# Kernel tuning notes

Hardware: AMD Instinct MI355X
Metric: run time of the kernel (lower is better)

Reference implementation:

```python
import jax, jax.numpy as jnp
import numpy as np

N_POOL = 500_000   # number of source neurons (value store size)
N_W = 1024         # number of unique (deduplicated) weight matrices
E = 1_000_000      # number of connections (neuron-input pairs)
D_IN = 16
D_OUT = 16


def setup_inputs() -> dict:
    key = jax.random.key(0)
    k1, k2, k3, k4 = jax.random.split(key, 4)
    values = jax.random.normal(k1, (N_POOL, D_IN), dtype=jnp.float32)
    weight = jax.random.normal(k2, (N_W, D_OUT, D_IN), dtype=jnp.float32)
    input_idx = jax.random.randint(k3, (E,), 0, N_POOL, dtype=jnp.int64) if jax.config.jax_enable_x64 else jax.random.randint(k3, (E,), 0, N_POOL).astype(jnp.int32)
    weight_idx = jax.random.randint(k4, (E,), 0, N_W).astype(jnp.int32)
    return {"values": values, "weight": weight, "input_idx": input_idx, "weight_idx": weight_idx}


def reference(values, weight, input_idx, weight_idx):
    # LINEAR_GATHER: gather input value vectors per connection  -> [E, D_IN]
    x = values[input_idx]
    # LINEAR_WEIGHTS_GATHER: gather weight matrices per connection -> [E, D_OUT, D_IN]
    w = weight[weight_idx]
    # LINEAR_LINEAR: per-connection matmul (w @ input_values) -> [E, D_OUT]
    y = jnp.einsum('eoi,ei->eo', w, x)
    return y
```

## Files before the change

### kernel.cpp

```cpp
#include <hip/hip_runtime.h>
#include <hip/hip_fp16.h>


#define D 16
#define WPB 4
#define TPB (WPB * 64)
#define MAXBLK 2048

typedef _Float16 h2v __attribute__((ext_vector_type(2)));

__global__ __launch_bounds__(256) void linear_gather_mv(
    const float* __restrict__ values, const float* __restrict__ weight,
    const int* __restrict__ input_idx, const int* __restrict__ weight_idx,
    float* __restrict__ out, int E)
{
    int tid = blockIdx.x * blockDim.x + threadIdx.x;
    int e = tid >> 2;
    int j = tid & 3;
    if (e >= E) return;
    int ii = input_idx[e];
    int wi = weight_idx[e];
    const float4* xp = (const float4*)(values + (long long)ii * D);
    float4 x0 = xp[0], x1 = xp[1], x2 = xp[2], x3 = xp[3];
    const float4* wp = (const float4*)(weight + (long long)wi * (D * D) + j * (4 * D));
    float4 acc;
    float* accp = (float*)&acc;
    #pragma unroll
    for (int r = 0; r < 4; ++r) {
        float4 w0 = wp[r * 4 + 0], w1 = wp[r * 4 + 1], w2 = wp[r * 4 + 2], w3 = wp[r * 4 + 3];
        accp[r] = w0.x * x0.x + w0.y * x0.y + w0.z * x0.z + w0.w * x0.w
                + w1.x * x1.x + w1.y * x1.y + w1.z * x1.z + w1.w * x1.w
                + w2.x * x2.x + w2.y * x2.y + w2.z * x2.z + w2.w * x2.w
                + w3.x * x3.x + w3.y * x3.y + w3.z * x3.z + w3.w * x3.w;
    }
    ((float4*)out)[(long long)e * 4 + j] = acc;
}

__global__ __launch_bounds__(256) void wconv(
    const float* __restrict__ w, __half* __restrict__ wh, int n)
{
    int i = (blockIdx.x * 256 + threadIdx.x) * 4;
    if (i + 3 >= n) {
        for (int k = i; k < n; ++k) wh[k] = __float2half(w[k]);
        return;
    }
    float4 v = *(const float4*)(w + i);
    __half2 a = __floats2half2_rn(v.x, v.y);
    __half2 b = __floats2half2_rn(v.z, v.w);
    float2 packed;
    ((__half2*)&packed)[0] = a;
    ((__half2*)&packed)[1] = b;
    *(float2*)(wh + i) = packed;
}

#define WPAIR(K, W0, W1) do {                                                  \
    int a0 = __builtin_amdgcn_readlane(wcur, 4*(K)+0);                         \
    int a1 = __builtin_amdgcn_readlane(wcur, 4*(K)+1);                         \
    int a2 = __builtin_amdgcn_readlane(wcur, 4*(K)+2);                         \
    int a3 = __builtin_amdgcn_readlane(wcur, 4*(K)+3);                         \
    W0 = ((const float4*)(wh + (long long)(lh ? a1 : a0) * (D*D)))[hrow];      \
    W1 = ((const float4*)(wh + (long long)(lh ? a3 : a2) * (D*D)))[hrow];      \
} while (0)

#define STEP(CC, WV) do {                                                      \
    int c  = (CC) + lh;                                                        \
    float4 xv = *(const float4*)(xh + (size_t)c * D + (h << 3));               \
    const h2v* xp2 = (const h2v*)&xv;                                          \
    const h2v* wp2 = (const h2v*)&(WV);                                        \
    float p = __builtin_amdgcn_fdot2(wp2[0], xp2[0], 0.0f, false);             \
    p = __builtin_amdgcn_fdot2(wp2[1], xp2[1], p, false);                      \
    p = __builtin_amdgcn_fdot2(wp2[2], xp2[2], p, false);                      \
    p = __builtin_amdgcn_fdot2(wp2[3], xp2[3], p, false);                      \
    p += __shfl_xor(p, 1);            \
    if (h == 0) yh[c * D + rr] = (_Float16)p;                                  \
} while (0)

#define COMP4(K, W0, W1) do { STEP(4*(K)+0, W0); STEP(4*(K)+2, W1); } while (0)

#define IDXLOAD(BI, IV, WV) do {                                               \
    int kl = (BI) * 64 + lane; if (kl >= E) kl = E - 1;                        \
    IV = iidx[kl];                                                             \
    WV = widx[kl];                                                             \
} while (0)

#define XLOAD(IV) do {                                                         \
    int iiu;                                                                   \
    iiu = __shfl(IV,      g4); xq0 = ((const float4*)(values + (long long)iiu * D))[q]; \
    iiu = __shfl(IV, 16 + g4); xq1 = ((const float4*)(values + (long long)iiu * D))[q]; \
    iiu = __shfl(IV, 32 + g4); xq2 = ((const float4*)(values + (long long)iiu * D))[q]; \
    iiu = __shfl(IV, 48 + g4); xq3 = ((const float4*)(values + (long long)iiu * D))[q]; \
} while (0)

#define COMMIT(U, XQ) do {                                                     \
    __half2 c0 = __floats2half2_rn((XQ).x, (XQ).y);                            \
    __half2 c1 = __floats2half2_rn((XQ).z, (XQ).w);                            \
    float2 pk;                                                                 \
    ((__half2*)&pk)[0] = c0;                                                   \
    ((__half2*)&pk)[1] = c1;                                                   \
    *(float2*)(xh + ((U)*16 + g4) * D + (q << 2)) = pk;                        \
} while (0)

__global__ __launch_bounds__(TPB, 4) void direct_mv(
    const float* __restrict__ values, const __half* __restrict__ wh,
    const int* __restrict__ iidx, const int* __restrict__ widx,
    float* __restrict__ out, int E)
{
    __shared__ _Float16 xh_all[WPB * 64 * D];
    __shared__ _Float16 yh_all[WPB * 64 * D];
    const int lane = threadIdx.x & 63;
    const int wid  = threadIdx.x >> 6;
    _Float16* xh = xh_all + wid * (64 * D);
    _Float16* yh = yh_all + wid * (64 * D);
    const int g4 = lane >> 2;
    const int q  = lane & 3;
    const int lh   = lane >> 5;
    const int h    = lane & 1;
    const int hrow = lane & 31;
    const int rr   = (lane & 31) >> 1;

    const int nbatch = (E + 63) >> 6;
    const int gw = blockIdx.x * WPB + wid;
    const int GW = gridDim.x * WPB;
    if (gw >= nbatch) return;

    int ivC, wvC, ivN, wvN;
    float4 xq0, xq1, xq2, xq3;
    IDXLOAD(gw, ivC, wvC);
    XLOAD(ivC);
    if (gw + GW < nbatch) IDXLOAD(gw + GW, ivN, wvN);
    else { ivN = ivC; wvN = wvC; }

    for (int bi = gw; bi < nbatch; bi += GW) {
        COMMIT(0, xq0);
        COMMIT(1, xq1);
        COMMIT(2, xq2);
        COMMIT(3, xq3);
        int wcur = wvC;
        int k0 = bi * 64;
        int nb = E - k0; if (nb > 64) nb = 64;
        float* outb = out + (long long)k0 * D;

        int bn = bi + GW;
        if (bn < nbatch) XLOAD(ivN);
        int bn2 = bi + 2 * GW;
        if (bn2 < nbatch) IDXLOAD(bn2, ivC, wvC);

        float4 P0, P1, Q0, Q1;
        WPAIR( 0, P0, P1);
        WPAIR( 1, Q0, Q1);
        COMP4( 0, P0, P1); WPAIR( 2, P0, P1);
        COMP4( 1, Q0, Q1); WPAIR( 3, Q0, Q1);
        COMP4( 2, P0, P1); WPAIR( 4, P0, P1);
        COMP4( 3, Q0, Q1); WPAIR( 5, Q0, Q1);
        COMP4( 4, P0, P1); WPAIR( 6, P0, P1);
        COMP4( 5, Q0, Q1); WPAIR( 7, Q0, Q1);
        COMP4( 6, P0, P1); WPAIR( 8, P0, P1);
        COMP4( 7, Q0, Q1); WPAIR( 9, Q0, Q1);
        COMP4( 8, P0, P1); WPAIR(10, P0, P1);
        COMP4( 9, Q0, Q1); WPAIR(11, Q0, Q1);
        COMP4(10, P0, P1); WPAIR(12, P0, P1);
        COMP4(11, Q0, Q1); WPAIR(13, Q0, Q1);
        COMP4(12, P0, P1); WPAIR(14, P0, P1);
        COMP4(13, Q0, Q1); WPAIR(15, Q0, Q1);
        COMP4(14, P0, P1);
        COMP4(15, Q0, Q1);

        #pragma unroll
        for (int j = 0; j < 4; ++j) {
            float2 raw = *(const float2*)((const char*)yh + j * 512 + lane * 8);
            float2 f0 = __half22float2(((const __half2*)&raw)[0]);
            float2 f1 = __half22float2(((const __half2*)&raw)[1]);
            float4 o;
            o.x = f0.x; o.y = f0.y; o.z = f1.x; o.w = f1.y;
            int cc = j * 16 + (lane >> 2);
            if (cc < nb)
                *(float4*)(outb + (size_t)j * 256 + lane * 4) = o;
        }

        int t;
        t = ivC; ivC = ivN; ivN = t;
        t = wvC; wvC = wvN; wvN = t;
    }
}

extern "C" void kernel_launch(void* const* d_in, const int* in_sizes, int n_in,
                              void* d_out, int out_size, void* d_ws, size_t ws_size,
                              hipStream_t stream) {
    const float* values     = (const float*)d_in[0];
    const float* weight     = (const float*)d_in[1];
    const int*   input_idx  = (const int*)d_in[2];
    const int*   weight_idx = (const int*)d_in[3];
    float*       out        = (float*)d_out;

    int E = in_sizes[2];
    if (E <= 0) return;
    int NW = in_sizes[1] / (D * D);
    size_t need = (size_t)NW * D * D * sizeof(__half);

    if (ws_size < need) {
        int total_thr = E * 4;
        int grid = (total_thr + 255) / 256;
        hipLaunchKernelGGL(linear_gather_mv, dim3(grid), dim3(256), 0, stream,
                           values, weight, input_idx, weight_idx, out, E);
        return;
    }

    __half* wh = (__half*)d_ws;
    int nconv = NW * D * D;
    int cblk = (nconv / 4 + 255) / 256;
    hipLaunchKernelGGL(wconv, dim3(cblk), dim3(256), 0, stream,
                       weight, wh, nconv);

    int nbatch = (E + 63) >> 6;
    int nblk = (nbatch + WPB - 1) / WPB;
    if (nblk > MAXBLK) nblk = MAXBLK;
    hipLaunchKernelGGL(direct_mv, dim3(nblk), dim3(TPB), 0, stream,
                       values, wh, input_idx, weight_idx, out, E);
}
```

Before: 124.5 us.

## Software-pipeline weight and gather loads with inline asm and manual vmcnt waits

Replaces compiler-generated global loads with inline-asm dwordx4 loads and explicit s_waitcnt vmcnt counters. Weight matrices now go through a four-slot register ring, so more loads are in flight at once. The next batch's weight and value loads are issued during the tail of the current batch. Output conversion and stores are deferred one iteration through a double-buffered LDS result area, so the stores overlap compute. The aim is to hide gather latency in this memory-bound kernel, at the cost of more registers and LDS and fragile hand-counted wait values that may over-wait or break correctness if the counts are wrong.

Result: slower. 128.6 us (+3.3%).

```diff
diff --git a/kernel.cpp b/kernel.cpp
--- a/kernel.cpp
+++ b/kernel.cpp
@@ -7,7 +7,8 @@
 #define TPB (WPB * 64)
 #define MAXBLK 2048
 
-typedef _Float16 h2v __attribute__((ext_vector_type(2)));
+typedef float    f32x4 __attribute__((ext_vector_type(4)));
+typedef _Float16 h2v   __attribute__((ext_vector_type(2)));
 
 __global__ __launch_bounds__(256) void linear_gather_mv(
     const float* __restrict__ values, const float* __restrict__ weight,
@@ -53,42 +54,55 @@
     *(float2*)(wh + i) = packed;
 }
 
-#define WPAIR(K, W0, W1) do {                                                  \
-    int a0 = __builtin_amdgcn_readlane(wcur, 4*(K)+0);                         \
-    int a1 = __builtin_amdgcn_readlane(wcur, 4*(K)+1);                         \
-    int a2 = __builtin_amdgcn_readlane(wcur, 4*(K)+2);                         \
-    int a3 = __builtin_amdgcn_readlane(wcur, 4*(K)+3);                         \
-    W0 = ((const float4*)(wh + (long long)(lh ? a1 : a0) * (D*D)))[hrow];      \
-    W1 = ((const float4*)(wh + (long long)(lh ? a3 : a2) * (D*D)))[hrow];      \
-} while (0)
+#define WISSUE(WIV, K, W0, W1) do {                                            \
+    int a0 = __builtin_amdgcn_readlane(WIV, 4*(K)+0);                          \
+    int a1 = __builtin_amdgcn_readlane(WIV, 4*(K)+1);                          \
+    int a2 = __builtin_amdgcn_readlane(WIV, 4*(K)+2);                          \
+    int a3 = __builtin_amdgcn_readlane(WIV, 4*(K)+3);                          \
+    unsigned long long ad0 = wb + ((unsigned long long)(unsigned)(lh ? a1 : a0) << 9); \
+    unsigned long long ad1 = wb + ((unsigned long long)(unsigned)(lh ? a3 : a2) << 9); \
+    asm volatile("global_load_dwordx4 %0, %2, off\n\t"                         \
+                 "global_load_dwordx4 %1, %3, off"                             \
+                 : "=&v"(W0), "=&v"(W1)                                        \
+                 : "v"(ad0), "v"(ad1) : "memory");                             \
+} while (0)
+
+#define VWAIT(N, W0, W1)                                                       \
+    asm volatile("s_waitcnt vmcnt(" #N ")" : "+v"(W0), "+v"(W1))
 
 #define STEP(CC, WV) do {                                                      \
     int c  = (CC) + lh;                                                        \
-    float4 xv = *(const float4*)(xh + (size_t)c * D + (h << 3));               \
+    f32x4 xv = *(const f32x4*)(xh + (size_t)c * D + (h << 3));                 \
     const h2v* xp2 = (const h2v*)&xv;                                          \
     const h2v* wp2 = (const h2v*)&(WV);                                        \
     float p = __builtin_amdgcn_fdot2(wp2[0], xp2[0], 0.0f, false);             \
     p = __builtin_amdgcn_fdot2(wp2[1], xp2[1], p, false);                      \
     p = __builtin_amdgcn_fdot2(wp2[2], xp2[2], p, false);                      \
     p = __builtin_amdgcn_fdot2(wp2[3], xp2[3], p, false);                      \
-    p += __shfl_xor(p, 1);            \
-    if (h == 0) yh[c * D + rr] = (_Float16)p;                                  \
+    p += __shfl_xor(p, 1);                                                     \
+    if (h == 0) yw[c * D + rr] = (_Float16)p;                                  \
 } while (0)
 
 #define COMP4(K, W0, W1) do { STEP(4*(K)+0, W0); STEP(4*(K)+2, W1); } while (0)
 
-#define IDXLOAD(BI, IV, WV) do {                                               \
+#define IDXA(BI, IV, WV) do {                                                  \
     int kl = (BI) * 64 + lane; if (kl >= E) kl = E - 1;                        \
-    IV = iidx[kl];                                                             \
-    WV = widx[kl];                                                             \
-} while (0)
-
-#define XLOAD(IV) do {                                                         \
-    int iiu;                                                                   \
-    iiu = __shfl(IV,      g4); xq0 = ((const float4*)(values + (long long)iiu * D))[q]; \
-    iiu = __shfl(IV, 16 + g4); xq1 = ((const float4*)(values + (long long)iiu * D))[q]; \
-    iiu = __shfl(IV, 32 + g4); xq2 = ((const float4*)(values + (long long)iiu * D))[q]; \
-    iiu = __shfl(IV, 48 + g4); xq3 = ((const float4*)(values + (long long)iiu * D))[q]; \
+    unsigned long long ai = (unsigned long long)iidx + ((unsigned)kl << 2);    \
+    unsigned long long aw = (unsigned long long)widx + ((unsigned)kl << 2);    \
+    asm volatile("global_load_dword %0, %1, off" : "=&v"(IV) : "v"(ai) : "memory"); \
+    asm volatile("global_load_dword %0, %1, off" : "=&v"(WV) : "v"(aw) : "memory"); \
+} while (0)
+
+#define XLOADA(IV) do {                                                        \
+    int iiu; unsigned long long ax;                                            \
+    iiu = __shfl(IV,      g4); ax = vb + ((unsigned long long)(unsigned)iiu << 6); \
+    asm volatile("global_load_dwordx4 %0, %1, off" : "=&v"(xq0) : "v"(ax) : "memory"); \
+    iiu = __shfl(IV, 16 + g4); ax = vb + ((unsigned long long)(unsigned)iiu << 6); \
+    asm volatile("global_load_dwordx4 %0, %1, off" : "=&v"(xq1) : "v"(ax) : "memory"); \
+    iiu = __shfl(IV, 32 + g4); ax = vb + ((unsigned long long)(unsigned)iiu << 6); \
+    asm volatile("global_load_dwordx4 %0, %1, off" : "=&v"(xq2) : "v"(ax) : "memory"); \
+    iiu = __shfl(IV, 48 + g4); ax = vb + ((unsigned long long)(unsigned)iiu << 6); \
+    asm volatile("global_load_dwordx4 %0, %1, off" : "=&v"(xq3) : "v"(ax) : "memory"); \
 } while (0)
 
 #define COMMIT(U, XQ) do {                                                     \
@@ -100,17 +114,36 @@
     *(float2*)(xh + ((U)*16 + g4) * D + (q << 2)) = pk;                        \
 } while (0)
 
+#define DRAIN(YD, PO, PNB) do {                                                \
+    _Pragma("unroll")                                                          \
+    for (int j = 0; j < 4; ++j) {                                              \
+        float2 raw = *(const float2*)((const char*)(YD) + j * 512 + lane * 8); \
+        float2 f0 = __half22float2(((const __half2*)&raw)[0]);                 \
+        float2 f1 = __half22float2(((const __half2*)&raw)[1]);                 \
+        f32x4 o; o.x = f0.x; o.y = f0.y; o.z = f1.x; o.w = f1.y;               \
+        int cc = j * 16 + (lane >> 2);                                         \
+        if (cc < (PNB)) {                                                      \
+            unsigned long long ao = (unsigned long long)(PO)                   \
+                                  + (unsigned)(j * 1024 + lane * 16);          \
+            asm volatile("global_store_dwordx4 %0, %1, off"                    \
+                         :: "v"(ao), "v"(o) : "memory");                       \
+        }                                                                      \
+    }                                                                          \
+} while (0)
+
 __global__ __launch_bounds__(TPB, 4) void direct_mv(
     const float* __restrict__ values, const __half* __restrict__ wh,
     const int* __restrict__ iidx, const int* __restrict__ widx,
     float* __restrict__ out, int E)
 {
     __shared__ _Float16 xh_all[WPB * 64 * D];
-    __shared__ _Float16 yh_all[WPB * 64 * D];
+    __shared__ _Float16 yA_all[WPB * 64 * D];
+    __shared__ _Float16 yB_all[WPB * 64 * D];
     const int lane = threadIdx.x & 63;
     const int wid  = threadIdx.x >> 6;
     _Float16* xh = xh_all + wid * (64 * D);
-    _Float16* yh = yh_all + wid * (64 * D);
+    _Float16* yA = yA_all + wid * (64 * D);
+    _Float16* yB = yB_all + wid * (64 * D);
     const int g4 = lane >> 2;
     const int q  = lane & 3;
     const int lh   = lane >> 5;
@@ -118,69 +151,83 @@
     const int hrow = lane & 31;
     const int rr   = (lane & 31) >> 1;
 
+    const unsigned long long wb = (unsigned long long)wh + (unsigned)(hrow << 4);
+    const unsigned long long vb = (unsigned long long)values + (unsigned)(q << 4);
+
     const int nbatch = (E + 63) >> 6;
     const int gw = blockIdx.x * WPB + wid;
     const int GW = gridDim.x * WPB;
     if (gw >= nbatch) return;
 
     int ivC, wvC, ivN, wvN;
-    float4 xq0, xq1, xq2, xq3;
-    IDXLOAD(gw, ivC, wvC);
-    XLOAD(ivC);
-    if (gw + GW < nbatch) IDXLOAD(gw + GW, ivN, wvN);
+    f32x4 xq0, xq1, xq2, xq3;
+    f32x4 A0, A1, B0, B1, C0, C1, E0, E1;
+
+    IDXA(gw, ivC, wvC);
+    asm volatile("s_waitcnt vmcnt(0)" : "+v"(ivC), "+v"(wvC));
+    XLOADA(ivC);
+    if (gw + GW < nbatch) IDXA(gw + GW, ivN, wvN);
     else { ivN = ivC; wvN = wvC; }
+    WISSUE(wvC, 0, A0, A1);
+    WISSUE(wvC, 1, B0, B1);
+    WISSUE(wvC, 2, C0, C1);
+    WISSUE(wvC, 3, E0, E1);
+    VWAIT(6, A0, A1);
+
+    float* po = nullptr; int pnb = 0;
+    _Float16* yw = yA;
+    _Float16* yd = yB;
 
     for (int bi = gw; bi < nbatch; bi += GW) {
+        asm volatile("s_waitcnt vmcnt(6)"
+                     : "+v"(xq0), "+v"(xq1), "+v"(xq2), "+v"(xq3),
+                       "+v"(A0), "+v"(A1),
+                       "+v"(wvC), "+v"(ivN), "+v"(wvN));
         COMMIT(0, xq0);
         COMMIT(1, xq1);
         COMMIT(2, xq2);
         COMMIT(3, xq3);
-        int wcur = wvC;
+        if (po) DRAIN(yd, po, pnb);
         int k0 = bi * 64;
         int nb = E - k0; if (nb > 64) nb = 64;
-        float* outb = out + (long long)k0 * D;
+
+        COMP4( 0, A0, A1);                   WISSUE(wvC,  4, A0, A1);
+        VWAIT(6, B0, B1); COMP4( 1, B0, B1); WISSUE(wvC,  5, B0, B1);
+        VWAIT(6, C0, C1); COMP4( 2, C0, C1); WISSUE(wvC,  6, C0, C1);
+        VWAIT(6, E0, E1); COMP4( 3, E0, E1); WISSUE(wvC,  7, E0, E1);
+        VWAIT(6, A0, A1); COMP4( 4, A0, A1); WISSUE(wvC,  8, A0, A1);
+        VWAIT(6, B0, B1); COMP4( 5, B0, B1); WISSUE(wvC,  9, B0, B1);
+        VWAIT(6, C0, C1); COMP4( 6, C0, C1); WISSUE(wvC, 10, C0, C1);
+        VWAIT(6, E0, E1); COMP4( 7, E0, E1); WISSUE(wvC, 11, E0, E1);
+        VWAIT(6, A0, A1); COMP4( 8, A0, A1); WISSUE(wvC, 12, A0, A1);
+        VWAIT(6, B0, B1); COMP4( 9, B0, B1); WISSUE(wvC, 13, B0, B1);
+        VWAIT(6, C0, C1); COMP4(10, C0, C1); WISSUE(wvC, 14, C0, C1);
+        VWAIT(6, E0, E1); COMP4(11, E0, E1); WISSUE(wvC, 15, E0, E1);
+        VWAIT(6, A0, A1); COMP4(12, A0, A1);
 
         int bn = bi + GW;
-        if (bn < nbatch) XLOAD(ivN);
-        int bn2 = bi + 2 * GW;
-        if (bn2 < nbatch) IDXLOAD(bn2, ivC, wvC);
-
-        float4 P0, P1, Q0, Q1;
-        WPAIR( 0, P0, P1);
-        WPAIR( 1, Q0, Q1);
-        COMP4( 0, P0, P1); WPAIR( 2, P0, P1);
-        COMP4( 1, Q0, Q1); WPAIR( 3, Q0, Q1);
-        COMP4( 2, P0, P1); WPAIR( 4, P0, P1);
-        COMP4( 3, Q0, Q1); WPAIR( 5, Q0, Q1);
-        COMP4( 4, P0, P1); WPAIR( 6, P0, P1);
-        COMP4( 5, Q0, Q1); WPAIR( 7, Q0, Q1);
-        COMP4( 6, P0, P1); WPAIR( 8, P0, P1);
-        COMP4( 7, Q0, Q1); WPAIR( 9, Q0, Q1);
-        COMP4( 8, P0, P1); WPAIR(10, P0, P1);
-        COMP4( 9, Q0, Q1); WPAIR(11, Q0, Q1);
-        COMP4(10, P0, P1); WPAIR(12, P0, P1);
-        COMP4(11, Q0, Q1); WPAIR(13, Q0, Q1);
-        COMP4(12, P0, P1); WPAIR(14, P0, P1);
-        COMP4(13, Q0, Q1); WPAIR(15, Q0, Q1);
-        COMP4(14, P0, P1);
-        COMP4(15, Q0, Q1);
-
-        #pragma unroll
-        for (int j = 0; j < 4; ++j) {
-            float2 raw = *(const float2*)((const char*)yh + j * 512 + lane * 8);
-            float2 f0 = __half22float2(((const __half2*)&raw)[0]);
-            float2 f1 = __half22float2(((const __half2*)&raw)[1]);
-            float4 o;
-            o.x = f0.x; o.y = f0.y; o.z = f1.x; o.w = f1.y;
-            int cc = j * 16 + (lane >> 2);
-            if (cc < nb)
-                *(float4*)(outb + (size_t)j * 256 + lane * 4) = o;
+        if (bn < nbatch) {
+            WISSUE(wvN, 0, A0, A1);
+            XLOADA(ivN);
+            int bn2 = bi + 2 * GW;
+            if (bn2 < nbatch) IDXA(bn2, ivC, wvC);
+            VWAIT(10, B0, B1); COMP4(13, B0, B1); WISSUE(wvN, 1, B0, B1);
+            VWAIT(10, C0, C1); COMP4(14, C0, C1); WISSUE(wvN, 2, C0, C1);
+            VWAIT(10, E0, E1); COMP4(15, E0, E1); WISSUE(wvN, 3, E0, E1);
+        } else {
+            VWAIT(4, B0, B1); COMP4(13, B0, B1);
+            VWAIT(2, C0, C1); COMP4(14, C0, C1);
+            VWAIT(0, E0, E1); COMP4(15, E0, E1);
         }
 
+        po = out + (long long)k0 * D; pnb = nb;
         int t;
         t = ivC; ivC = ivN; ivN = t;
         t = wvC; wvC = wvN; wvN = t;
-    }
+        _Float16* ty = yw; yw = yd; yd = ty;
+    }
+
+    if (po) DRAIN(yd, po, pnb);
 }
 
 extern "C" void kernel_launch(void* const* d_in, const int* in_sizes, int n_in,
```
